# Kernel optimization log

Hardware: AMD Instinct MI355X
Metric: run time of the kernel (lower is better)

## Reference

```python
import jax, jax.numpy as jnp
import numpy as np

N_GRAPHS = 4
NODES_PER_GRAPH = 8192
N_NODES = N_GRAPHS * NODES_PER_GRAPH
N_EDGES = N_NODES * 16
IN_DIM = 3
HID = 128
K_OUT = 512
MAX_WAVELENGTH = 10000.0


def _glorot(k, shape):
    lim = (6.0 / (shape[0] + shape[1])) ** 0.5
    return jax.random.uniform(k, shape, jnp.float32, -lim, lim)


def setup_inputs() -> dict:
    key = jax.random.key(0)
    ks = jax.random.split(key, 12)
    z = lambda *s: jnp.zeros(s, jnp.float32)
    return {
        "x": jax.random.normal(ks[0], (N_NODES, IN_DIM), jnp.float32),
        "mesh_pos": jax.random.uniform(ks[1], (N_NODES, 2), jnp.float32),
        "mesh_edges": jax.random.randint(ks[2], (N_EDGES, 2), 0, N_NODES, jnp.int32),
        "batch_idx": jnp.arange(N_NODES, dtype=jnp.int32) // NODES_PER_GRAPH,
        "proj_w": _glorot(ks[3], (IN_DIM, HID)), "proj_b": z(HID),
        "msg_w1": _glorot(ks[4], (2 * HID, HID)), "msg_b1": z(HID),
        "msg_w2": _glorot(ks[5], (HID, HID)), "msg_b2": z(HID),
        "upd_w1": _glorot(ks[6], (2 * HID, HID)), "upd_b1": z(HID),
        "upd_w2": _glorot(ks[7], (HID, HID)), "upd_b2": z(HID),
        "pool_rel_w": _glorot(ks[8], (HID, 1)), "pool_rel_b": z(1),
        "pool_root_w": _glorot(ks[9], (HID, 1)),
    }


def _sincos_embed(pos):
    # ContinuousSincosEmbed: HID=128, ndim=2 -> 64 channels per coord dim, 32 freqs
    dim_per_ndim = HID // 2
    omega = 1.0 / MAX_WAVELENGTH ** (jnp.arange(0, dim_per_ndim, 2, dtype=jnp.float32) / dim_per_ndim)
    ang = pos[:, :, None] * omega  # [N, ndim, 32]
    emb = jnp.concatenate([jnp.sin(ang), jnp.cos(ang)], axis=-1)  # [N, ndim, 64]
    return emb.reshape(pos.shape[0], HID)


def reference(x, mesh_pos, mesh_edges, batch_idx, proj_w, proj_b,
              msg_w1, msg_b1, msg_w2, msg_b2, upd_w1, upd_b1, upd_w2, upd_b2,
              pool_rel_w, pool_rel_b, pool_root_w):
    src, dst = mesh_edges[:, 0], mesh_edges[:, 1]  # edge_index[0]=j(src), [1]=i(dst)
    h = x @ proj_w + proj_b + _sincos_embed(mesh_pos)
    cnt = jnp.maximum(jax.ops.segment_sum(jnp.ones((N_EDGES,), h.dtype), dst, num_segments=N_NODES), 1.0)
    # message passing layer (depth=1): message MLP on [x_i, x_j], scatter-mean, residual update MLP
    m_in = jnp.concatenate([h[dst], h[src]], axis=-1)  # [E, 2H]
    m = jax.nn.silu(m_in @ msg_w1 + msg_b1) @ msg_w2 + msg_b2
    agg = jax.ops.segment_sum(m, dst, num_segments=N_NODES) / cnt[:, None]
    h = h + (jax.nn.silu(jnp.concatenate([h, agg], axis=-1) @ upd_w1 + upd_b1) @ upd_w2 + upd_b2)
    # SAGPooling score: GraphConv(HID,1,aggr='mean'), tanh nonlinearity
    nagg = jax.ops.segment_sum(h[src], dst, num_segments=N_NODES) / cnt[:, None]
    score = jnp.tanh((nagg @ pool_rel_w + pool_rel_b + h @ pool_root_w)[:, 0])
    # fixed top-k per graph (batch_idx is contiguous blocks of NODES_PER_GRAPH)
    topv, topi = jax.lax.top_k(score.reshape(N_GRAPHS, NODES_PER_GRAPH), K_OUT)
    perm = (topi + jnp.arange(N_GRAPHS, dtype=topi.dtype)[:, None] * NODES_PER_GRAPH).reshape(-1)
    x_pool = h[perm] * topv.reshape(-1)[:, None]
    batch_pool = jnp.repeat(jnp.arange(N_GRAPHS, dtype=batch_idx.dtype), K_OUT)
    return x_pool, batch_pool
```

## Files before the change

### kernel.cpp

```cpp
#include <hip/hip_runtime.h>
#include <hip/hip_bf16.h>
#include <math.h>

#define N_NODESC 32768
#define N_EDGESC 524288
#define NPG 8192
#define KOUT 512

typedef unsigned short u16;
typedef unsigned int u32;
typedef unsigned long long u64;

__device__ __forceinline__ float siluf(float x) {
    return x / (1.f + __expf(-x));
}

__global__ __launch_bounds__(256) void k_h0(const float* __restrict__ x,
                                            const float* __restrict__ pos,
                                            const float* __restrict__ pw,
                                            const float* __restrict__ pb,
                                            float* __restrict__ h,
                                            int* __restrict__ deg) {
    int gid = blockIdx.x * 256 + threadIdx.x;
    if (gid < N_NODESC) deg[gid] = 0;
    int node = blockIdx.x * 2 + (threadIdx.x >> 7);
    int c = threadIdx.x & 127;
    float x0 = x[node * 3 + 0];
    float x1 = x[node * 3 + 1];
    float x2 = x[node * 3 + 2];
    float acc = x0 * pw[c] + x1 * pw[128 + c] + x2 * pw[256 + c];
    acc += pb[c];
    int dim = c >> 6;
    int inner = c & 63;
    int jj = inner & 31;
    float p = pos[node * 2 + dim];
    float omega = exp2f(-(float)jj * 0.41524101186092027f);
    float ang = p * omega;
    acc += (inner < 32) ? __sinf(ang) : __cosf(ang);
    h[(size_t)node * 128 + c] = acc;
}

__global__ __launch_bounds__(256) void k_deg(const int* __restrict__ edges, int* __restrict__ deg) {
    int e = blockIdx.x * 256 + threadIdx.x;
    if (e < N_EDGESC) {
        int2 e2 = ((const int2*)edges)[e];
        atomicAdd(&deg[e2.y], 1);
    }
}

__global__ __launch_bounds__(1024) void k_scan(const int* __restrict__ deg,
                                               int* __restrict__ off, int* __restrict__ cur,
                                               float* __restrict__ rs, float* __restrict__ bg) {
    __shared__ int ls[1024];
    int tid = threadIdx.x;
    int base = tid * 32;
    int v[32];
    int s = 0;
#pragma unroll
    for (int j = 0; j < 32; j++) { v[j] = deg[base + j]; s += v[j]; }
    ls[tid] = s;
    __syncthreads();
    for (int ofs = 1; ofs < 1024; ofs <<= 1) {
        int t = (tid >= ofs) ? ls[tid - ofs] : 0;
        __syncthreads();
        ls[tid] += t;
        __syncthreads();
    }
    int run = ls[tid] - s;
#pragma unroll
    for (int j = 0; j < 32; j++) {
        off[base + j] = run;
        cur[base + j] = run;
        int d = v[j];
        rs[base + j] = 1.f / (float)(d > 0 ? d : 1);
        bg[base + j] = d > 0 ? 1.f : 0.f;
        run += d;
    }
}

__global__ __launch_bounds__(256) void k_fill(const int* __restrict__ edges,
                                              int* __restrict__ cur, int* __restrict__ csr) {
    int e = blockIdx.x * 256 + threadIdx.x;
    if (e < N_EDGESC) {
        int2 e2 = ((const int2*)edges)[e];
        int pos = atomicAdd(&cur[e2.y], 1);
        csr[pos] = e2.x;
    }
}

__global__ __launch_bounds__(256) void k_sortcsr(int* __restrict__ csr,
                                                 const int* __restrict__ off,
                                                 const int* __restrict__ deg) {
    int d = blockIdx.x * 4 + (threadIdx.x >> 6);
    int lane = threadIdx.x & 63;
    int o = off[d], n = deg[d];
    if (n <= 1) return;
    if (n <= 64) {
        int key = (lane < n) ? csr[o + lane] : 0x7FFFFFFF;
        for (int k = 2; k <= 64; k <<= 1) {
            for (int j = k >> 1; j > 0; j >>= 1) {
                int partner = __shfl_xor(key, j);
                bool asc = ((lane & k) == 0);
                bool keepMin = (((lane & j) == 0) == asc);
                key = keepMin ? min(key, partner) : max(key, partner);
            }
        }
        if (lane < n) csr[o + lane] = key;
    } else {
        if (lane == 0) {
            for (int i = o + 1; i < o + n; i++) {
                int x = csr[i];
                int j = i - 1;
                while (j >= o && csr[j] > x) { csr[j + 1] = csr[j]; j--; }
                csr[j + 1] = x;
            }
        }
    }
}

__global__ __launch_bounds__(256, 2) void gemm_lds(const float* __restrict__ A, const float* __restrict__ W,
                                                   const float* __restrict__ bias,
                                                   const float* __restrict__ rs, const float* __restrict__ bg,
                                                   const float* __restrict__ resid,
                                                   float* __restrict__ C, int act,
                                                   const float* __restrict__ wrel, const float* __restrict__ wroot,
                                                   float* __restrict__ pout, float* __restrict__ rout) {
    __shared__ float Ws[32 * 128];
    int tid = threadIdx.x;
    int cg = tid & 31;
    int rg = tid >> 5;
    int m0 = blockIdx.x * 32 + rg * 4;
    int c0 = cg * 4;
    const float* Ar = A + (size_t)m0 * 128;

    float acc[4][4];
#pragma unroll
    for (int r = 0; r < 4; r++)
#pragma unroll
        for (int c = 0; c < 4; c++) acc[r][c] = 0.f;

    float4 aA[4], aB[4], wA[4], wB[4];

#define LOAD_A(buf, k)                                                   \
    {                                                                    \
        _Pragma("unroll") for (int r = 0; r < 4; r++)                    \
            buf[r] = *(const float4*)(Ar + r * 128 + (k));               \
    }
#define LOAD_W(buf, k)                                                   \
    {                                                                    \
        _Pragma("unroll") for (int kk = 0; kk < 4; kk++)                 \
            buf[kk] = *(const float4*)(Ws + ((k) + kk) * 128 + c0);      \
    }
#define COMPUTE(ab, wb)                                                  \
    {                                                                    \
        _Pragma("unroll") for (int kk = 0; kk < 4; kk++) {               \
            float4 wv = wb[kk];                                          \
            _Pragma("unroll") for (int r = 0; r < 4; r++) {              \
                float a = ((const float*)&ab[r])[kk];                    \
                acc[r][0] += a * wv.x;                                   \
                acc[r][1] += a * wv.y;                                   \
                acc[r][2] += a * wv.z;                                   \
                acc[r][3] += a * wv.w;                                   \
            }                                                            \
        }                                                                \
    }

    for (int kc = 0; kc < 128; kc += 32) {
        __syncthreads();
        {
            const float4* Wg = (const float4*)(W + (size_t)kc * 128);
            float4* Wl = (float4*)Ws;
#pragma unroll
            for (int i = 0; i < 4; i++) Wl[tid + i * 256] = Wg[tid + i * 256];
        }
        __syncthreads();
        LOAD_A(aA, kc)
        LOAD_W(wA, 0)
        for (int k0 = 0; k0 < 32; k0 += 8) {
            LOAD_A(aB, kc + k0 + 4)
            LOAD_W(wB, k0 + 4)
            COMPUTE(aA, wA)
            if (k0 + 8 < 32) {
                LOAD_A(aA, kc + k0 + 8)
                LOAD_W(wA, k0 + 8)
            }
            COMPUTE(aB, wB)
        }
    }
#undef LOAD_A
#undef LOAD_W
#undef COMPUTE

    float prel[4], prot[4];
#pragma unroll
    for (int r = 0; r < 4; r++) {
        int row = m0 + r;
        float rsv = rs ? rs[row] : 1.f;
        float bgv = bg ? bg[row] : 1.f;
        float4 o;
        float* op = (float*)&o;
#pragma unroll
        for (int c = 0; c < 4; c++) {
            float xv = acc[r][c];
            xv *= rsv;
            if (bias) xv += bias[c0 + c] * bgv;
            if (resid) xv += resid[(size_t)row * 128 + c0 + c];
            if (act) xv = siluf(xv);
            op[c] = xv;
        }
        if (wrel) {
            prel[r] = op[0] * wrel[c0] + op[1] * wrel[c0 + 1] + op[2] * wrel[c0 + 2] + op[3] * wrel[c0 + 3];
            prot[r] = op[0] * wroot[c0] + op[1] * wroot[c0 + 1] + op[2] * wroot[c0 + 2] + op[3] * wroot[c0 + 3];
        }
        *(float4*)(C + (size_t)row * 128 + c0) = o;
    }
    if (wrel) {
#pragma unroll
        for (int r = 0; r < 4; r++) {
            float a = prel[r], b = prot[r];
#pragma unroll
            for (int m = 1; m < 32; m <<= 1) {
                a += __shfl_xor(a, m);
                b += __shfl_xor(b, m);
            }
            if (cg == 0) { pout[m0 + r] = a; rout[m0 + r] = b; }
        }
    }
}

__global__ __launch_bounds__(256) void k_accum_S(const float* __restrict__ v,
                                                 const int* __restrict__ csr, const int* __restrict__ off,
                                                 const int* __restrict__ deg, float* S) {
    int d = blockIdx.x * 4 + (threadIdx.x >> 6);
    int lane = threadIdx.x & 63;
    float* srow = S + (size_t)d * 128;
    float u0 = srow[lane];
    float u1 = srow[64 + lane];
    float a0 = 0.f, a1 = 0.f;
    int o = off[d], n = deg[d];
    for (int base = 0; base < n; base += 64) {
        int cnt = min(64, n - base);
        int sall = (lane < cnt) ? csr[o + base + lane] : 0;
        int j = 0;
        for (; j + 8 <= cnt; j += 8) {
            int s0 = __shfl(sall, j + 0), s1 = __shfl(sall, j + 1);
            int s2 = __shfl(sall, j + 2), s3 = __shfl(sall, j + 3);
            int s4 = __shfl(sall, j + 4), s5 = __shfl(sall, j + 5);
            int s6 = __shfl(sall, j + 6), s7 = __shfl(sall, j + 7);
            float v00 = v[(size_t)s0 * 128 + lane], v01 = v[(size_t)s0 * 128 + 64 + lane];
            float v10 = v[(size_t)s1 * 128 + lane], v11 = v[(size_t)s1 * 128 + 64 + lane];
            float v20 = v[(size_t)s2 * 128 + lane], v21 = v[(size_t)s2 * 128 + 64 + lane];
            float v30 = v[(size_t)s3 * 128 + lane], v31 = v[(size_t)s3 * 128 + 64 + lane];
            float v40 = v[(size_t)s4 * 128 + lane], v41 = v[(size_t)s4 * 128 + 64 + lane];
            float v50 = v[(size_t)s5 * 128 + lane], v51 = v[(size_t)s5 * 128 + 64 + lane];
            float v60 = v[(size_t)s6 * 128 + lane], v61 = v[(size_t)s6 * 128 + 64 + lane];
            float v70 = v[(size_t)s7 * 128 + lane], v71 = v[(size_t)s7 * 128 + 64 + lane];
            a0 += siluf(u0 + v00); a1 += siluf(u1 + v01);
            a0 += siluf(u0 + v10); a1 += siluf(u1 + v11);
            a0 += siluf(u0 + v20); a1 += siluf(u1 + v21);
            a0 += siluf(u0 + v30); a1 += siluf(u1 + v31);
            a0 += siluf(u0 + v40); a1 += siluf(u1 + v41);
            a0 += siluf(u0 + v50); a1 += siluf(u1 + v51);
            a0 += siluf(u0 + v60); a1 += siluf(u1 + v61);
            a0 += siluf(u0 + v70); a1 += siluf(u1 + v71);
        }
        for (; j < cnt; j++) {
            int s = __shfl(sall, j);
            a0 += siluf(u0 + v[(size_t)s * 128 + lane]);
            a1 += siluf(u1 + v[(size_t)s * 128 + 64 + lane]);
        }
    }
    srow[lane] = a0;
    srow[64 + lane] = a1;
}

__global__ __launch_bounds__(256) void k_score(const float* __restrict__ p, const float* __restrict__ r,
                                               const int* __restrict__ csr, const int* __restrict__ off,
                                               const int* __restrict__ deg, const float* __restrict__ relb,
                                               float* __restrict__ score) {
    int d = blockIdx.x * 4 + (threadIdx.x >> 6);
    int lane = threadIdx.x & 63;
    int o = off[d], n = deg[d];
    float a = 0.f;
    for (int j = lane; j < n; j += 64) a += p[csr[o + j]];
    for (int m = 32; m > 0; m >>= 1) a += __shfl_xor(a, m);
    if (lane == 0) {
        float cnt = (float)(n > 0 ? n : 1);
        score[d] = tanhf(a / cnt + relb[0] + r[d]);
    }
}

__global__ __launch_bounds__(1024) void k_topk(const float* __restrict__ score, const float* __restrict__ h,
                                               float* __restrict__ out) {
    __shared__ u32 ms[NPG];
    __shared__ u32 hist[256];
    __shared__ u32 sbuf[1024];
    __shared__ u64 sel[KOUT];
    __shared__ float ordv[KOUT];
    __shared__ int ordi[KOUT];
    __shared__ u32 selCnt, sPrefix, sNeed, sB;

    int g = blockIdx.x;
    int tid = threadIdx.x;

    for (int i = tid; i < NPG; i += 1024) {
        u32 u = __float_as_uint(score[(size_t)g * NPG + i]);
        ms[i] = (u & 0x80000000u) ? ~u : (u | 0x80000000u);
    }
    if (tid == 0) { sNeed = KOUT; sPrefix = 0; selCnt = 0; }
    __syncthreads();

    for (int pass = 0; pass < 4; pass++) {
        int shift = 24 - pass * 8;
        if (tid < 256) hist[tid] = 0;
        __syncthreads();
        u32 pfx = sPrefix;
        for (int i = tid; i < NPG; i += 1024) {
            u32 v = ms[i];
            if (pass == 0 || (v >> (shift + 8)) == pfx)
                atomicAdd(&hist[(v >> shift) & 255u], 1u);
        }
        __syncthreads();
        if (tid < 256) sbuf[tid] = hist[tid];
        __syncthreads();
        for (int ofs = 1; ofs < 256; ofs <<= 1) {
            u32 t = 0;
            if (tid < 256 && tid + ofs < 256) t = sbuf[tid + ofs];
            __syncthreads();
            if (tid < 256) sbuf[tid] += t;
            __syncthreads();
        }
        u32 need = sNeed;
        if (tid < 256) {
            if (sbuf[tid] >= need && (tid == 255 || sbuf[tid + 1] < need)) sB = (u32)tid;
        }
        __syncthreads();
        if (tid == 0) {
            u32 B = sB;
            u32 above = (B == 255) ? 0u : sbuf[B + 1];
            sNeed = need - above;
            sPrefix = (sPrefix << 8) | B;
        }
        __syncthreads();
    }
    u32 T = sPrefix;
    u32 rTie = sNeed;

    int base = tid * 8;
    u32 lc = 0;
#pragma unroll
    for (int j = 0; j < 8; j++) lc += (ms[base + j] == T);
    __syncthreads();
    sbuf[tid] = lc;
    __syncthreads();
    u32 own = lc;
    for (int ofs = 1; ofs < 1024; ofs <<= 1) {
        u32 t = (tid >= ofs) ? sbuf[tid - ofs] : 0;
        __syncthreads();
        sbuf[tid] += t;
        __syncthreads();
    }
    u32 excl = sbuf[tid] - own;

#pragma unroll
    for (int j = 0; j < 8; j++) {
        int i = base + j;
        u32 v = ms[i];
        bool pick = (v > T) || ((v == T) && (excl < rTie));
        if (v == T) excl++;
        if (pick) {
            u32 slot = atomicAdd(&selCnt, 1u);
            sel[slot] = ((u64)v << 32) | (u32)(NPG - 1 - i);
        }
    }
    __syncthreads();

    if (tid < KOUT) {
        u64 mine = sel[tid];
        int rank = 0;
        for (int j = 0; j < KOUT; j++) rank += (sel[j] > mine);
        u32 v = (u32)(mine >> 32);
        int idx = NPG - 1 - (int)(mine & 0xFFFFFFFFu);
        u32 uu = (v & 0x80000000u) ? (v & 0x7FFFFFFFu) : ~v;
        ordv[rank] = __uint_as_float(uu);
        ordi[rank] = idx;
    }
    __syncthreads();

    for (int t = tid; t < KOUT * 128; t += 1024) {
        int r = t >> 7, c = t & 127;
        int node = g * NPG + ordi[r];
        out[((size_t)g * KOUT + r) * 128 + c] = h[(size_t)node * 128 + c] * ordv[r];
    }
    for (int t = tid; t < KOUT; t += 1024)
        out[(size_t)4 * KOUT * 128 + (size_t)g * KOUT + t] = (float)g;
}

extern "C" void kernel_launch(void* const* d_in, const int* in_sizes, int n_in,
                              void* d_out, int out_size, void* d_ws, size_t ws_size,
                              hipStream_t stream) {
    const float* x        = (const float*)d_in[0];
    const float* mesh_pos = (const float*)d_in[1];
    const int*   edges    = (const int*)d_in[2];
    const float* proj_w   = (const float*)d_in[4];
    const float* proj_b   = (const float*)d_in[5];
    const float* msg_w1   = (const float*)d_in[6];
    const float* msg_b1   = (const float*)d_in[7];
    const float* msg_w2   = (const float*)d_in[8];
    const float* msg_b2   = (const float*)d_in[9];
    const float* upd_w1   = (const float*)d_in[10];
    const float* upd_b1   = (const float*)d_in[11];
    const float* upd_w2   = (const float*)d_in[12];
    const float* upd_b2   = (const float*)d_in[13];
    const float* pool_rel_w  = (const float*)d_in[14];
    const float* pool_rel_b  = (const float*)d_in[15];
    const float* pool_root_w = (const float*)d_in[16];
    float* out = (float*)d_out;

    char* w = (char*)d_ws;
    float* h  = (float*)(w);
    float* v  = (float*)(w + (1ull << 24));
    float* S  = (float*)(w + (2ull << 24));
    char* sm  = w + (3ull << 24);
    int*   deg   = (int*)(sm);
    int*   off   = (int*)(sm + 131072);
    int*   cur   = (int*)(sm + 262144);
    float* rsA   = (float*)(sm + 393216);
    float* bgA   = (float*)(sm + 524288);
    float* pp    = (float*)(sm + 655360);
    float* rr    = (float*)(sm + 786432);
    float* score = (float*)(sm + 917504);
    int*   csr   = (int*)(sm + 1048576);

    k_h0<<<N_NODESC / 2, 256, 0, stream>>>(x, mesh_pos, proj_w, proj_b, h, deg);
    k_deg<<<N_EDGESC / 256, 256, 0, stream>>>(edges, deg);
    k_scan<<<1, 1024, 0, stream>>>(deg, off, cur, rsA, bgA);
    k_fill<<<N_EDGESC / 256, 256, 0, stream>>>(edges, cur, csr);
    k_sortcsr<<<N_NODESC / 4, 256, 0, stream>>>(csr, off, deg);

    gemm_lds<<<1024, 256, 0, stream>>>(h, msg_w1 + 128 * 128, nullptr, nullptr, nullptr, nullptr,
                                       v, 0, nullptr, nullptr, nullptr, nullptr);
    gemm_lds<<<1024, 256, 0, stream>>>(h, msg_w1, msg_b1, nullptr, nullptr, nullptr,
                                       S, 0, nullptr, nullptr, nullptr, nullptr);
    k_accum_S<<<N_NODESC / 4, 256, 0, stream>>>(v, csr, off, deg, S);
    gemm_lds<<<1024, 256, 0, stream>>>(S, msg_w2, msg_b2, rsA, bgA, nullptr,
                                       v, 0, nullptr, nullptr, nullptr, nullptr);
    gemm_lds<<<1024, 256, 0, stream>>>(h, upd_w1, upd_b1, nullptr, nullptr, nullptr,
                                       S, 0, nullptr, nullptr, nullptr, nullptr);
    gemm_lds<<<1024, 256, 0, stream>>>(v, upd_w1 + 128 * 128, nullptr, nullptr, nullptr, S,
                                       v, 1, nullptr, nullptr, nullptr, nullptr);
    gemm_lds<<<1024, 256, 0, stream>>>(v, upd_w2, upd_b2, nullptr, nullptr, h,
                                       h, 0, pool_rel_w, pool_root_w, pp, rr);

    k_score<<<N_NODESC / 4, 256, 0, stream>>>(pp, rr, csr, off, deg, pool_rel_b, score);
    k_topk<<<4, 1024, 0, stream>>>(score, h, out);
}
```

Before: 418.8 us.

## Fuse paired GEMMs into dual-weight kernels and vectorize edge accumulation

Replaces two separate GEMMs over the same input h (message W1 halves) with one kernel that loads A once and produces both outputs. It also merges the two update-MLP first-layer GEMMs into one kernel that sums both products, adds bias and applies SiLU, which removes an intermediate write and read of S. The per-destination edge accumulation now uses float4 loads, with each wave half processing alternate neighbors and a final cross-half shuffle reduction. The cost is doubled LDS and register use per block, which may reduce occupancy.

Result: faster. 393.5 us (-6.0%).

```diff
diff --git a/kernel.cpp b/kernel.cpp
--- a/kernel.cpp
+++ b/kernel.cpp
@@ -118,6 +118,150 @@
     }
 }
 
+__global__ __launch_bounds__(256, 2) void gemm_dualw(const float* __restrict__ A,
+                                                     const float* __restrict__ Wv,
+                                                     const float* __restrict__ Wu,
+                                                     const float* __restrict__ bu,
+                                                     float* __restrict__ V, float* __restrict__ U) {
+    __shared__ float Wsv[32 * 128];
+    __shared__ float Wsu[32 * 128];
+    int tid = threadIdx.x;
+    int cg = tid & 31;
+    int rg = tid >> 5;
+    int m0 = blockIdx.x * 32 + rg * 4;
+    int c0 = cg * 4;
+    const float* Ar = A + (size_t)m0 * 128;
+
+    float accv[4][4], accu[4][4];
+#pragma unroll
+    for (int r = 0; r < 4; r++)
+#pragma unroll
+        for (int c = 0; c < 4; c++) { accv[r][c] = 0.f; accu[r][c] = 0.f; }
+
+    for (int kc = 0; kc < 128; kc += 32) {
+        __syncthreads();
+        {
+            const float4* Wgv = (const float4*)(Wv + (size_t)kc * 128);
+            const float4* Wgu = (const float4*)(Wu + (size_t)kc * 128);
+            float4* Wlv = (float4*)Wsv;
+            float4* Wlu = (float4*)Wsu;
+#pragma unroll
+            for (int i = 0; i < 4; i++) {
+                Wlv[tid + i * 256] = Wgv[tid + i * 256];
+                Wlu[tid + i * 256] = Wgu[tid + i * 256];
+            }
+        }
+        __syncthreads();
+#pragma unroll
+        for (int k0 = 0; k0 < 32; k0 += 4) {
+            float4 a[4];
+#pragma unroll
+            for (int r = 0; r < 4; r++) a[r] = *(const float4*)(Ar + r * 128 + kc + k0);
+#pragma unroll
+            for (int kk = 0; kk < 4; kk++) {
+                float4 wv = *(const float4*)(Wsv + (k0 + kk) * 128 + c0);
+                float4 wu = *(const float4*)(Wsu + (k0 + kk) * 128 + c0);
+#pragma unroll
+                for (int r = 0; r < 4; r++) {
+                    float aa = ((const float*)&a[r])[kk];
+                    accv[r][0] += aa * wv.x; accv[r][1] += aa * wv.y;
+                    accv[r][2] += aa * wv.z; accv[r][3] += aa * wv.w;
+                    accu[r][0] += aa * wu.x; accu[r][1] += aa * wu.y;
+                    accu[r][2] += aa * wu.z; accu[r][3] += aa * wu.w;
+                }
+            }
+        }
+    }
+#pragma unroll
+    for (int r = 0; r < 4; r++) {
+        int row = m0 + r;
+        float4 ov, ou;
+        ov.x = accv[r][0]; ov.y = accv[r][1]; ov.z = accv[r][2]; ov.w = accv[r][3];
+        ou.x = accu[r][0] + bu[c0];
+        ou.y = accu[r][1] + bu[c0 + 1];
+        ou.z = accu[r][2] + bu[c0 + 2];
+        ou.w = accu[r][3] + bu[c0 + 3];
+        *(float4*)(V + (size_t)row * 128 + c0) = ov;
+        *(float4*)(U + (size_t)row * 128 + c0) = ou;
+    }
+}
+
+__global__ __launch_bounds__(256, 2) void gemm_dualA(const float* __restrict__ A1,
+                                                     const float* __restrict__ W1,
+                                                     const float* __restrict__ A2,
+                                                     const float* __restrict__ W2,
+                                                     const float* __restrict__ bias,
+                                                     float* __restrict__ C) {
+    __shared__ float Ws1[32 * 128];
+    __shared__ float Ws2[32 * 128];
+    int tid = threadIdx.x;
+    int cg = tid & 31;
+    int rg = tid >> 5;
+    int m0 = blockIdx.x * 32 + rg * 4;
+    int c0 = cg * 4;
+    const float* Ar1 = A1 + (size_t)m0 * 128;
+    const float* Ar2 = A2 + (size_t)m0 * 128;
+
+    float acc1[4][4], acc2[4][4];
+#pragma unroll
+    for (int r = 0; r < 4; r++)
+#pragma unroll
+        for (int c = 0; c < 4; c++) { acc1[r][c] = 0.f; acc2[r][c] = 0.f; }
+
+    for (int kc = 0; kc < 128; kc += 32) {
+        __syncthreads();
+        {
+            const float4* Wg1 = (const float4*)(W1 + (size_t)kc * 128);
+            const float4* Wg2 = (const float4*)(W2 + (size_t)kc * 128);
+            float4* Wl1 = (float4*)Ws1;
+            float4* Wl2 = (float4*)Ws2;
+#pragma unroll
+            for (int i = 0; i < 4; i++) {
+                Wl1[tid + i * 256] = Wg1[tid + i * 256];
+                Wl2[tid + i * 256] = Wg2[tid + i * 256];
+            }
+        }
+        __syncthreads();
+#pragma unroll
+        for (int k0 = 0; k0 < 32; k0 += 4) {
+            float4 a1[4], a2[4];
+#pragma unroll
+            for (int r = 0; r < 4; r++) {
+                a1[r] = *(const float4*)(Ar1 + r * 128 + kc + k0);
+                a2[r] = *(const float4*)(Ar2 + r * 128 + kc + k0);
+            }
+#pragma unroll
+            for (int kk = 0; kk < 4; kk++) {
+                float4 w1 = *(const float4*)(Ws1 + (k0 + kk) * 128 + c0);
+                float4 w2 = *(const float4*)(Ws2 + (k0 + kk) * 128 + c0);
+#pragma unroll
+                for (int r = 0; r < 4; r++) {
+                    float aa = ((const float*)&a1[r])[kk];
+                    float bb = ((const float*)&a2[r])[kk];
+                    acc1[r][0] += aa * w1.x; acc1[r][1] += aa * w1.y;
+                    acc1[r][2] += aa * w1.z; acc1[r][3] += aa * w1.w;
+                    acc2[r][0] += bb * w2.x; acc2[r][1] += bb * w2.y;
+                    acc2[r][2] += bb * w2.z; acc2[r][3] += bb * w2.w;
+                }
+            }
+        }
+    }
+#pragma unroll
+    for (int r = 0; r < 4; r++) {
+        int row = m0 + r;
+        float4 o;
+        float* op = (float*)&o;
+#pragma unroll
+        for (int c = 0; c < 4; c++) {
+            float xv = acc1[r][c];
+            xv += acc2[r][c];
+            xv += bias[c0 + c];
+            op[c] = siluf(xv);
+        }
+        *(float4*)(C + (size_t)row * 128 + c0) = o;
+    }
+}
+
 __global__ __launch_bounds__(256, 2) void gemm_lds(const float* __restrict__ A, const float* __restrict__ W,
                                                    const float* __restrict__ bias,
                                                    const float* __restrict__ rs, const float* __restrict__ bg,
@@ -233,45 +377,59 @@
                                                  const int* __restrict__ deg, float* S) {
     int d = blockIdx.x * 4 + (threadIdx.x >> 6);
     int lane = threadIdx.x & 63;
+    int half = lane >> 5;
+    int l32 = lane & 31;
     float* srow = S + (size_t)d * 128;
-    float u0 = srow[lane];
-    float u1 = srow[64 + lane];
-    float a0 = 0.f, a1 = 0.f;
+    float4 u = *(const float4*)(srow + l32 * 4);
+    float4 a = {0.f, 0.f, 0.f, 0.f};
     int o = off[d], n = deg[d];
     for (int base = 0; base < n; base += 64) {
         int cnt = min(64, n - base);
         int sall = (lane < cnt) ? csr[o + base + lane] : 0;
         int j = 0;
         for (; j + 8 <= cnt; j += 8) {
-            int s0 = __shfl(sall, j + 0), s1 = __shfl(sall, j + 1);
-            int s2 = __shfl(sall, j + 2), s3 = __shfl(sall, j + 3);
-            int s4 = __shfl(sall, j + 4), s5 = __shfl(sall, j + 5);
-            int s6 = __shfl(sall, j + 6), s7 = __shfl(sall, j + 7);
-            float v00 = v[(size_t)s0 * 128 + lane], v01 = v[(size_t)s0 * 128 + 64 + lane];
-            float v10 = v[(size_t)s1 * 128 + lane], v11 = v[(size_t)s1 * 128 + 64 + lane];
-            float v20 = v[(size_t)s2 * 128 + lane], v21 = v[(size_t)s2 * 128 + 64 + lane];
-            float v30 = v[(size_t)s3 * 128 + lane], v31 = v[(size_t)s3 * 128 + 64 + lane];
-            float v40 = v[(size_t)s4 * 128 + lane], v41 = v[(size_t)s4 * 128 + 64 + lane];
-            float v50 = v[(size_t)s5 * 128 + lane], v51 = v[(size_t)s5 * 128 + 64 + lane];
-            float v60 = v[(size_t)s6 * 128 + lane], v61 = v[(size_t)s6 * 128 + 64 + lane];
-            float v70 = v[(size_t)s7 * 128 + lane], v71 = v[(size_t)s7 * 128 + 64 + lane];
-            a0 += siluf(u0 + v00); a1 += siluf(u1 + v01);
-            a0 += siluf(u0 + v10); a1 += siluf(u1 + v11);
-            a0 += siluf(u0 + v20); a1 += siluf(u1 + v21);
-            a0 += siluf(u0 + v30); a1 += siluf(u1 + v31);
-            a0 += siluf(u0 + v40); a1 += siluf(u1 + v41);
-            a0 += siluf(u0 + v50); a1 += siluf(u1 + v51);
-            a0 += siluf(u0 + v60); a1 += siluf(u1 + v61);
-            a0 += siluf(u0 + v70); a1 += siluf(u1 + v71);
-        }
-        for (; j < cnt; j++) {
-            int s = __shfl(sall, j);
-            a0 += siluf(u0 + v[(size_t)s * 128 + lane]);
-            a1 += siluf(u1 + v[(size_t)s * 128 + 64 + lane]);
-        }
-    }
-    srow[lane] = a0;
-    srow[64 + lane] = a1;
+            int s0 = __shfl(sall, j + 0 + half);
+            int s1 = __shfl(sall, j + 2 + half);
+            int s2 = __shfl(sall, j + 4 + half);
+            int s3 = __shfl(sall, j + 6 + half);
+            float4 v0 = *(const float4*)(v + (size_t)s0 * 128 + l32 * 4);
+            float4 v1 = *(const float4*)(v + (size_t)s1 * 128 + l32 * 4);
+            float4 v2 = *(const float4*)(v + (size_t)s2 * 128 + l32 * 4);
+            float4 v3 = *(const float4*)(v + (size_t)s3 * 128 + l32 * 4);
+            a.x += siluf(u.x + v0.x); a.y += siluf(u.y + v0.y);
+            a.z += siluf(u.z + v0.z); a.w += siluf(u.w + v0.w);
+            a.x += siluf(u.x + v1.x); a.y += siluf(u.y + v1.y);
+            a.z += siluf(u.z + v1.z); a.w += siluf(u.w + v1.w);
+            a.x += siluf(u.x + v2.x); a.y += siluf(u.y + v2.y);
+            a.z += siluf(u.z + v2.z); a.w += siluf(u.w + v2.w);
+            a.x += siluf(u.x + v3.x); a.y += siluf(u.y + v3.y);
+            a.z += siluf(u.z + v3.z); a.w += siluf(u.w + v3.w);
+        }
+        for (; j < cnt; j += 2) {
+            if (j + 1 < cnt) {
+                int s = __shfl(sall, j + half);
+                float4 vv = *(const float4*)(v + (size_t)s * 128 + l32 * 4);
+                a.x += siluf(u.x + vv.x); a.y += siluf(u.y + vv.y);
+                a.z += siluf(u.z + vv.z); a.w += siluf(u.w + vv.w);
+            } else {
+                int s = __shfl(sall, j);
+                if (half == 0) {
+                    float4 vv = *(const float4*)(v + (size_t)s * 128 + l32 * 4);
+                    a.x += siluf(u.x + vv.x); a.y += siluf(u.y + vv.y);
+                    a.z += siluf(u.z + vv.z); a.w += siluf(u.w + vv.w);
+                }
+            }
+        }
+    }
+    float ox = __shfl(a.x, l32 + 32);
+    float oy = __shfl(a.y, l32 + 32);
+    float oz = __shfl(a.z, l32 + 32);
+    float ow = __shfl(a.w, l32 + 32);
+    if (half == 0) {
+        float4 t;
+        t.x = a.x + ox; t.y = a.y + oy; t.z = a.z + oz; t.w = a.w + ow;
+        *(float4*)(srow + l32 * 4) = t;
+    }
 }
 
 __global__ __launch_bounds__(256) void k_score(const float* __restrict__ p, const float* __restrict__ r,
@@ -438,18 +596,12 @@
     k_fill<<<N_EDGESC / 256, 256, 0, stream>>>(edges, cur, csr);
     k_sortcsr<<<N_NODESC / 4, 256, 0, stream>>>(csr, off, deg);
 
-    gemm_lds<<<1024, 256, 0, stream>>>(h, msg_w1 + 128 * 128, nullptr, nullptr, nullptr, nullptr,
-                                       v, 0, nullptr, nullptr, nullptr, nullptr);
-    gemm_lds<<<1024, 256, 0, stream>>>(h, msg_w1, msg_b1, nullptr, nullptr, nullptr,
-                                       S, 0, nullptr, nullptr, nullptr, nullptr);
+    gemm_dualw<<<1024, 256, 0, stream>>>(h, msg_w1 + 128 * 128, msg_w1, msg_b1, v, S);
     k_accum_S<<<N_NODESC / 4, 256, 0, stream>>>(v, csr, off, deg, S);
     gemm_lds<<<1024, 256, 0, stream>>>(S, msg_w2, msg_b2, rsA, bgA, nullptr,
                                        v, 0, nullptr, nullptr, nullptr, nullptr);
-    gemm_lds<<<1024, 256, 0, stream>>>(h, upd_w1, upd_b1, nullptr, nullptr, nullptr,
-                                       S, 0, nullptr, nullptr, nullptr, nullptr);
-    gemm_lds<<<1024, 256, 0, stream>>>(v, upd_w1 + 128 * 128, nullptr, nullptr, nullptr, S,
-                                       v, 1, nullptr, nullptr, nullptr, nullptr);
-    gemm_lds<<<1024, 256, 0, stream>>>(v, upd_w2, upd_b2, nullptr, nullptr, h,
+    gemm_dualA<<<1024, 256, 0, stream>>>(h, upd_w1, v, upd_w1 + 128 * 128, upd_b1, S);
+    gemm_lds<<<1024, 256, 0, stream>>>(S, upd_w2, upd_b2, nullptr, nullptr, h,
                                        h, 0, pool_rel_w, pool_root_w, pp, rr);
 
     k_score<<<N_NODESC / 4, 256, 0, stream>>>(pp, rr, csr, off, deg, pool_rel_b, score);
```
